# Kernel optimization log

Measured on AMD Instinct MI355X. Metric: run time of the kernel, lower is better.

The kernel has to match this reference:

```python
import jax, jax.numpy as jnp
import numpy as np

N_NODES = 100000
IN_DIM = 64
HID = 128
HID2 = HID // 2
N_CLASSES = 2
N_EDGES = 1600000
BN_EPS = 1e-5


def setup_inputs() -> dict:
    key = jax.random.key(0)
    ks = jax.random.split(key, 12)
    x = jax.random.normal(ks[0], (N_NODES, IN_DIM), dtype=jnp.float32)
    edge_index = jax.random.randint(ks[1], (2, N_EDGES), 0, N_NODES, dtype=jnp.int64)
    s = lambda k, shp, fan: jax.random.normal(k, shp, dtype=jnp.float32) / np.sqrt(fan)
    return {
        "x": x,
        "edge_index": edge_index,
        # SAGEConv1: lin_l (on aggregated neighbors, has bias), lin_r (root, no bias)
        "W1_l": s(ks[2], (IN_DIM, HID), IN_DIM),
        "b1_l": jnp.zeros((HID,), jnp.float32),
        "W1_r": s(ks[3], (IN_DIM, HID), IN_DIM),
        # SAGEConv2
        "W2_l": s(ks[4], (HID, HID2), HID),
        "b2_l": jnp.zeros((HID2,), jnp.float32),
        "W2_r": s(ks[5], (HID, HID2), HID),
        # BatchNorm (eval mode: running stats)
        "bn1_gamma": jnp.ones((HID,), jnp.float32),
        "bn1_beta": jnp.zeros((HID,), jnp.float32),
        "bn1_mean": jax.random.normal(ks[6], (HID,), dtype=jnp.float32) * 0.1,
        "bn1_var": jax.random.uniform(ks[7], (HID,), minval=0.5, maxval=1.5, dtype=jnp.float32),
        "bn2_gamma": jnp.ones((HID2,), jnp.float32),
        "bn2_beta": jnp.zeros((HID2,), jnp.float32),
        "bn2_mean": jax.random.normal(ks[8], (HID2,), dtype=jnp.float32) * 0.1,
        "bn2_var": jax.random.uniform(ks[9], (HID2,), minval=0.5, maxval=1.5, dtype=jnp.float32),
        # classifier
        "Wc": s(ks[10], (HID2, N_CLASSES), HID2),
        "bc": jnp.zeros((N_CLASSES,), jnp.float32),
    }


def _sage_mean(h, src, dst, Wl, bl, Wr, n_nodes):
    # gather source-node features along edges, scatter-mean into destinations
    msg = h[src]                                            # [E, D]
    summed = jax.ops.segment_sum(msg, dst, num_segments=n_nodes)  # [N, D]
    cnt = jax.ops.segment_sum(jnp.ones_like(dst, dtype=h.dtype), dst, num_segments=n_nodes)
    mean = summed / jnp.maximum(cnt, 1.0)[:, None]
    return mean @ Wl + bl + h @ Wr


def _bn_eval(h, gamma, beta, mean, var):
    return (h - mean) * (gamma * jax.lax.rsqrt(var + BN_EPS)) + beta


def reference(x, edge_index, W1_l, b1_l, W1_r, W2_l, b2_l, W2_r,
              bn1_gamma, bn1_beta, bn1_mean, bn1_var,
              bn2_gamma, bn2_beta, bn2_mean, bn2_var, Wc, bc):
    src, dst = edge_index[0], edge_index[1]
    n = x.shape[0]
    h = _sage_mean(x, src, dst, W1_l, b1_l, W1_r, n)
    h = jax.nn.relu(_bn_eval(h, bn1_gamma, bn1_beta, bn1_mean, bn1_var))
    h = _sage_mean(h, src, dst, W2_l, b2_l, W2_r, n)
    h = jax.nn.relu(_bn_eval(h, bn2_gamma, bn2_beta, bn2_mean, bn2_var))
    return h @ Wc + bc  # logits [N, num_classes]
```

## Files before the change

### kernel.cpp

```cpp
#include <hip/hip_runtime.h>
#include <math.h>

#define N_NODES 100000
#define IN_DIM 64
#define HID 128
#define HID2 64
#define N_EDGES 1600000
#define BN_EPS 1e-5f

#define NPB 128
#define NB 782
#define BIN_BLOCKS 391
#define BIN_CHUNK 4096
#define SORT_CAP 4096

typedef __attribute__((ext_vector_type(8))) __bf16 bf16x8;
typedef __attribute__((ext_vector_type(4))) float f32x4;
typedef __attribute__((ext_vector_type(2))) float f32x2;
typedef __attribute__((ext_vector_type(8))) unsigned short u16x8;

__device__ __forceinline__ unsigned short f2bf(float f) {
    unsigned int u = __builtin_bit_cast(unsigned int, f);
    u += 0x7fffu + ((u >> 16) & 1u);
    return (unsigned short)(u >> 16);
}

__device__ __forceinline__ void accum_u2(float a[4], uint2 v) {
    a[0] += __builtin_bit_cast(float, v.x << 16);
    a[1] += __builtin_bit_cast(float, v.x);
    a[2] += __builtin_bit_cast(float, v.y << 16);
    a[3] += __builtin_bit_cast(float, v.y);
}

__device__ __forceinline__ void accum_fp8(float a[4], unsigned int u) {
    f32x2 lo = __builtin_amdgcn_cvt_pk_f32_fp8((int)u, false);
    f32x2 hi = __builtin_amdgcn_cvt_pk_f32_fp8((int)u, true);
    a[0] += lo.x; a[1] += lo.y; a[2] += hi.x; a[3] += hi.y;
}

__global__ __launch_bounds__(256) void prep_wfrag(
    const float* __restrict__ W1l, const float* __restrict__ W1r,
    const float* __restrict__ W2l, const float* __restrict__ W2r,
    unsigned short* __restrict__ Wf1, unsigned short* __restrict__ Wf2)
{
    int task = blockIdx.x * 4 + (threadIdx.x >> 6);
    int lane = threadIdx.x & 63;
    int m  = task >> 5;
    int nt = (task >> 2) & 7;
    int kt = task & 3;
    int col = nt * 16 + (lane & 15);
    int k0  = kt * 32 + (lane >> 4) * 8;
    unsigned short tmp[8];
    #pragma unroll
    for (int e = 0; e < 8; ++e) {
        int k = k0 + e;
        float v;
        if (m == 0) v = (k < 64) ? W1l[k * HID + col] : W1r[(k - 64) * HID + col];
        else        v = (col < 64) ? W2l[k * HID2 + col] : W2r[k * HID2 + (col - 64)];
        tmp[e] = f2bf(v);
    }
    unsigned short* dst = ((m == 0) ? Wf1 : Wf2)
                        + ((size_t)((nt * 4 + kt) * 64 + lane)) * 8;
    *(u16x8*)dst = *(const u16x8*)tmp;
}

__global__ __launch_bounds__(256) void cast_x(
    const float* __restrict__ x, unsigned short* __restrict__ Abuf)
{
    int tid = blockIdx.x * 256 + threadIdx.x;
    if (tid >= N_NODES * 16) return;
    int node = tid >> 4;
    int q    = tid & 15;
    float4 v = ((const float4*)x)[tid];
    unsigned short o[4] = {f2bf(v.x), f2bf(v.y), f2bf(v.z), f2bf(v.w)};
    *(uint2*)(Abuf + (size_t)node * 128 + 64 + q * 4) = *(const uint2*)o;
}

__global__ __launch_bounds__(256) void bin_count(
    const int* __restrict__ dst,
    int* __restrict__ bucketTotal,
    int* __restrict__ perBlockBase)
{
    __shared__ int cnt[NB];
    const int t = threadIdx.x;
    for (int i = t; i < NB; i += 256) cnt[i] = 0;
    __syncthreads();
    const int e0 = blockIdx.x * BIN_CHUNK;
    for (int i = t; i < BIN_CHUNK; i += 256) {
        int e = e0 + i;
        if (e < N_EDGES) atomicAdd(&cnt[dst[e] >> 7], 1);
    }
    __syncthreads();
    for (int b = t; b < NB; b += 256) {
        int c = cnt[b];
        if (c) perBlockBase[blockIdx.x * NB + b] = atomicAdd(&bucketTotal[b], c);
    }
}

__global__ __launch_bounds__(1024) void bucket_scan(
    const int* __restrict__ bucketTotal, int* __restrict__ bucketStart)
{
    __shared__ int s[1024];
    const int t = threadIdx.x;
    int v = (t < NB) ? bucketTotal[t] : 0;
    s[t] = v;
    __syncthreads();
    #pragma unroll
    for (int off = 1; off < 1024; off <<= 1) {
        int u = (t >= off) ? s[t - off] : 0;
        __syncthreads();
        s[t] += u;
        __syncthreads();
    }
    if (t < NB) bucketStart[t] = s[t] - v;
    if (t == 0) bucketStart[NB] = N_EDGES;
}

__global__ __launch_bounds__(256) void bin_write(
    const int* __restrict__ src, const int* __restrict__ dst,
    const int* __restrict__ bucketStart,
    const int* __restrict__ perBlockBase,
    unsigned int* __restrict__ binned)
{
    __shared__ int cur[NB];
    const int t = threadIdx.x;
    for (int i = t; i < NB; i += 256) cur[i] = 0;
    __syncthreads();
    const int e0 = blockIdx.x * BIN_CHUNK;
    for (int i = t; i < BIN_CHUNK; i += 256) {
        int e = e0 + i;
        if (e < N_EDGES) {
            int d = dst[e];
            int b = d >> 7;
            int pos = bucketStart[b] + perBlockBase[blockIdx.x * NB + b]
                    + atomicAdd(&cur[b], 1);
            binned[pos] = ((unsigned int)src[e] << 7) | (unsigned int)(d & 127);
        }
    }
}

__global__ __launch_bounds__(256) void bucket_sort(
    const unsigned int* __restrict__ binned,
    const int* __restrict__ bucketStart,
    int* __restrict__ sortedSrc,
    int* __restrict__ rowStart)
{
    __shared__ unsigned int stage[SORT_CAP];
    __shared__ int hist[NPB];
    __shared__ int cur[NPB];

    const int b  = blockIdx.x;
    const int t  = threadIdx.x;
    const int bs = bucketStart[b];
    const int be = bucketStart[b + 1];
    const int total = be - bs;

    if (t < NPB) hist[t] = 0;
    __syncthreads();

    if (total <= SORT_CAP) {
        for (int i = t; i < total; i += 256) {
            unsigned int p = binned[bs + i];
            stage[i] = p;
            atomicAdd(&hist[p & 127], 1);
        }
        __syncthreads();
        int orig = (t < NPB) ? hist[t] : 0;
        __syncthreads();
        #pragma unroll
        for (int off = 1; off < NPB; off <<= 1) {
            int v = (t < NPB && t >= off) ? hist[t - off] : 0;
            __syncthreads();
            if (t < NPB) hist[t] += v;
            __syncthreads();
        }
        if (t < NPB) {
            int excl = hist[t] - orig;
            int node = b * NPB + t;
            if (node < N_NODES) rowStart[node] = bs + excl;
            cur[t] = excl;
        }
        if (b == 0 && t == 0) rowStart[N_NODES] = N_EDGES;
        __syncthreads();
        for (int i = t; i < total; i += 256) {
            unsigned int p = stage[i];
            int pos = atomicAdd(&cur[p & 127], 1);
            sortedSrc[bs + pos] = (int)(p >> 7);
        }
    } else {
        for (int i = t; i < total; i += 256)
            atomicAdd(&hist[binned[bs + i] & 127], 1);
        __syncthreads();
        int orig = (t < NPB) ? hist[t] : 0;
        __syncthreads();
        #pragma unroll
        for (int off = 1; off < NPB; off <<= 1) {
            int v = (t < NPB && t >= off) ? hist[t - off] : 0;
            __syncthreads();
            if (t < NPB) hist[t] += v;
            __syncthreads();
        }
        if (t < NPB) {
            int excl = hist[t] - orig;
            int node = b * NPB + t;
            if (node < N_NODES) rowStart[node] = bs + excl;
            cur[t] = excl;
        }
        if (b == 0 && t == 0) rowStart[N_NODES] = N_EDGES;
        __syncthreads();
        for (int i = t; i < total; i += 256) {
            unsigned int p = binned[bs + i];
            int pos = atomicAdd(&cur[p & 127], 1);
            sortedSrc[bs + pos] = (int)(p >> 7);
        }
    }
}

__global__ __launch_bounds__(256) void gather1_q(
    const int* __restrict__ rowStart,
    const int* __restrict__ sortedSrc,
    unsigned short* __restrict__ Abuf)
{
    const int node = (int)((blockIdx.x * 256u + threadIdx.x) >> 4);
    const int lane = threadIdx.x & 63;
    const int q    = lane & 15;
    const int qb   = lane & 48;
    const int b = rowStart[node], e = rowStart[node + 1];

    float a0[4] = {0.f,0.f,0.f,0.f};
    float a1[4] = {0.f,0.f,0.f,0.f};
    float a2[4] = {0.f,0.f,0.f,0.f};
    float a3[4] = {0.f,0.f,0.f,0.f};

    for (int base = b; base < e; base += 16) {
        const int cnt = min(e - base, 16);
        int srcv = (base + q < e) ? sortedSrc[base + q] : 0;
        int i = 0;
        for (; i + 4 <= cnt; i += 4) {
            int s0 = __shfl(srcv, qb + i);
            int s1 = __shfl(srcv, qb + i + 1);
            int s2 = __shfl(srcv, qb + i + 2);
            int s3 = __shfl(srcv, qb + i + 3);
            accum_u2(a0, *(const uint2*)(Abuf + (size_t)s0 * 128 + 64 + q * 4));
            accum_u2(a1, *(const uint2*)(Abuf + (size_t)s1 * 128 + 64 + q * 4));
            accum_u2(a2, *(const uint2*)(Abuf + (size_t)s2 * 128 + 64 + q * 4));
            accum_u2(a3, *(const uint2*)(Abuf + (size_t)s3 * 128 + 64 + q * 4));
        }
        for (; i < cnt; ++i) {
            int s0 = __shfl(srcv, qb + i);
            accum_u2(a0, *(const uint2*)(Abuf + (size_t)s0 * 128 + 64 + q * 4));
        }
    }
    #pragma unroll
    for (int i = 0; i < 4; ++i) a0[i] = (a0[i] + a1[i]) + (a2[i] + a3[i]);

    float inv = 1.0f / fmaxf((float)(e - b), 1.0f);
    unsigned short o[4] = {f2bf(a0[0] * inv), f2bf(a0[1] * inv),
                           f2bf(a0[2] * inv), f2bf(a0[3] * inv)};
    *(uint2*)(Abuf + (size_t)node * 128 + q * 4) = *(const uint2*)o;
}

__global__ __launch_bounds__(256, 4) void gemm_fused_mfma(
    const unsigned short* __restrict__ Abuf,
    const unsigned short* __restrict__ Wf1,
    const unsigned short* __restrict__ Wf2,
    const float* __restrict__ b1l,
    const float* __restrict__ g1, const float* __restrict__ be1,
    const float* __restrict__ m1, const float* __restrict__ v1,
    const float* __restrict__ b2l,
    unsigned char* __restrict__ t1f8,
    unsigned short* __restrict__ r1bf)
{
    __shared__ unsigned short Al[64 * 136];

    const int t = threadIdx.x;
    const int w = t >> 6, l = t & 63;
    const int n0 = blockIdx.x * 64;

    {
        const int node = t >> 2, q = t & 3;
        const int nn = n0 + node;
        const uint4* srcp = (const uint4*)(Abuf + (size_t)nn * 128) + q * 4;
        uint4 z; z.x = z.y = z.z = z.w = 0u;
        unsigned short* drow = &Al[node * 136 + q * 32];
        #pragma unroll
        for (int i = 0; i < 4; ++i) {
            uint4 v = (nn < N_NODES) ? srcp[i] : z;
            *(uint4*)(drow + i * 8) = v;
        }
    }
    __syncthreads();

    const int row = l & 15, kq = l >> 4;

    f32x4 acc[4][2];
    #pragma unroll
    for (int a = 0; a < 4; ++a)
        #pragma unroll
        for (int b = 0; b < 2; ++b) acc[a][b] = (f32x4)(0.0f);

    #pragma unroll
    for (int kt = 0; kt < 4; ++kt) {
        bf16x8 bfr[2];
        #pragma unroll
        for (int n = 0; n < 2; ++n)
            bfr[n] = __builtin_bit_cast(bf16x8,
                *(const u16x8*)(Wf1 + ((size_t)(((2 * w + n) * 4 + kt) * 64 + l)) * 8));
        #pragma unroll
        for (int mt = 0; mt < 4; ++mt) {
            bf16x8 afr = __builtin_bit_cast(bf16x8,
                *(const u16x8*)&Al[(mt * 16 + row) * 136 + kt * 32 + kq * 8]);
            #pragma unroll
            for (int n = 0; n < 2; ++n)
                acc[mt][n] = __builtin_amdgcn_mfma_f32_16x16x32_bf16(
                    afr, bfr[n], acc[mt][n], 0, 0, 0);
        }
    }
    __syncthreads();

    #pragma unroll
    for (int n = 0; n < 2; ++n) {
        int j = w * 32 + n * 16 + (l & 15);
        float s  = g1[j] * rsqrtf(v1[j] + BN_EPS);
        float of = be1[j] + (b1l[j] - m1[j]) * s;
        #pragma unroll
        for (int mt = 0; mt < 4; ++mt) {
            #pragma unroll
            for (int i = 0; i < 4; ++i) {
                float h = fmaxf(fmaf(acc[mt][n][i], s, of), 0.0f);
                Al[(mt * 16 + kq * 4 + i) * 136 + j] = f2bf(h);
            }
        }
    }
    __syncthreads();

    f32x4 acc2[4][2];
    #pragma unroll
    for (int a = 0; a < 4; ++a)
        #pragma unroll
        for (int b = 0; b < 2; ++b) acc2[a][b] = (f32x4)(0.0f);

    #pragma unroll
    for (int kt = 0; kt < 4; ++kt) {
        bf16x8 bfr[2];
        #pragma unroll
        for (int n = 0; n < 2; ++n)
            bfr[n] = __builtin_bit_cast(bf16x8,
                *(const u16x8*)(Wf2 + ((size_t)(((2 * w + n) * 4 + kt) * 64 + l)) * 8));
        #pragma unroll
        for (int mt = 0; mt < 4; ++mt) {
            bf16x8 afr = __builtin_bit_cast(bf16x8,
                *(const u16x8*)&Al[(mt * 16 + row) * 136 + kt * 32 + kq * 8]);
            #pragma unroll
            for (int n = 0; n < 2; ++n)
                acc2[mt][n] = __builtin_amdgcn_mfma_f32_16x16x32_bf16(
                    afr, bfr[n], acc2[mt][n], 0, 0, 0);
        }
    }

    #pragma unroll
    for (int n = 0; n < 2; ++n) {
        int j = w * 32 + n * 16 + (l & 15);
        float bl = (w >= 2) ? b2l[j - 64] : 0.0f;
        #pragma unroll
        for (int mt = 0; mt < 4; ++mt) {
            #pragma unroll
            for (int i = 0; i < 4; ++i) {
                int node = n0 + mt * 16 + kq * 4 + i;
                if (node < N_NODES) {
                    float vv = acc2[mt][n][i];
                    if (w < 2) {
                        int p = __builtin_amdgcn_cvt_pk_fp8_f32(vv, vv, 0, false);
                        t1f8[(size_t)node * 64 + j] = (unsigned char)(p & 0xff);
                    } else {
                        r1bf[(size_t)node * 64 + (j - 64)] = f2bf(vv + bl);
                    }
                }
            }
        }
    }
}

__global__ __launch_bounds__(256) void gather2_q(
    const unsigned char* __restrict__ t1f8,
    const int* __restrict__ rowStart,
    const int* __restrict__ sortedSrc,
    const unsigned short* __restrict__ r1bf,
    const float* __restrict__ g2, const float* __restrict__ be2,
    const float* __restrict__ m2, const float* __restrict__ v2,
    const float* __restrict__ Wc, const float* __restrict__ bc,
    float* __restrict__ out)
{
    const int node = (int)((blockIdx.x * 256u + threadIdx.x) >> 4);
    const int lane = threadIdx.x & 63;
    const int q    = lane & 15;
    const int qb   = lane & 48;
    const int b = rowStart[node], e = rowStart[node + 1];

    float a0[4] = {0.f,0.f,0.f,0.f};
    float a1[4] = {0.f,0.f,0.f,0.f};
    float a2[4] = {0.f,0.f,0.f,0.f};
    float a3[4] = {0.f,0.f,0.f,0.f};

    for (int base = b; base < e; base += 16) {
        const int cnt = min(e - base, 16);
        int srcv = (base + q < e) ? sortedSrc[base + q] : 0;
        int i = 0;
        for (; i + 4 <= cnt; i += 4) {
            int s0 = __shfl(srcv, qb + i);
            int s1 = __shfl(srcv, qb + i + 1);
            int s2 = __shfl(srcv, qb + i + 2);
            int s3 = __shfl(srcv, qb + i + 3);
            accum_fp8(a0, *(const unsigned int*)(t1f8 + (size_t)s0 * 64 + q * 4));
            accum_fp8(a1, *(const unsigned int*)(t1f8 + (size_t)s1 * 64 + q * 4));
            accum_fp8(a2, *(const unsigned int*)(t1f8 + (size_t)s2 * 64 + q * 4));
            accum_fp8(a3, *(const unsigned int*)(t1f8 + (size_t)s3 * 64 + q * 4));
        }
        for (; i < cnt; ++i) {
            int s0 = __shfl(srcv, qb + i);
            accum_fp8(a0, *(const unsigned int*)(t1f8 + (size_t)s0 * 64 + q * 4));
        }
    }
    #pragma unroll
    for (int i = 0; i < 4; ++i) a0[i] = (a0[i] + a1[i]) + (a2[i] + a3[i]);

    const float inv = 1.0f / fmaxf((float)(e - b), 1.0f);
    const int f0 = q * 4;
    uint2 rv = *(const uint2*)(r1bf + (size_t)node * 64 + f0);
    float rr[4] = {
        __builtin_bit_cast(float, rv.x << 16),
        __builtin_bit_cast(float, rv.x & 0xffff0000u),
        __builtin_bit_cast(float, rv.y << 16),
        __builtin_bit_cast(float, rv.y & 0xffff0000u)
    };
    float l0 = 0.f, l1 = 0.f;
    #pragma unroll
    for (int i = 0; i < 4; ++i) {
        int f = f0 + i;
        float pre = a0[i] * inv + rr[i];
        float s   = g2[f] * rsqrtf(v2[f] + BN_EPS);
        float h2  = fmaxf((pre - m2[f]) * s + be2[f], 0.0f);
        l0 = fmaf(h2, Wc[f * 2 + 0], l0);
        l1 = fmaf(h2, Wc[f * 2 + 1], l1);
    }
    #pragma unroll
    for (int off = 8; off > 0; off >>= 1) {
        l0 += __shfl_xor(l0, off);
        l1 += __shfl_xor(l1, off);
    }
    if (q == 0) {
        out[(size_t)node * 2 + 0] = l0 + bc[0];
        out[(size_t)node * 2 + 1] = l1 + bc[1];
    }
}

extern "C" void kernel_launch(void* const* d_in, const int* in_sizes, int n_in,
                              void* d_out, int out_size, void* d_ws, size_t ws_size,
                              hipStream_t stream)
{
    const float* x    = (const float*)d_in[0];
    const int*   eidx = (const int*)d_in[1];
    const float* W1l  = (const float*)d_in[2];
    const float* b1l  = (const float*)d_in[3];
    const float* W1r  = (const float*)d_in[4];
    const float* W2l  = (const float*)d_in[5];
    const float* b2l  = (const float*)d_in[6];
    const float* W2r  = (const float*)d_in[7];
    const float* g1   = (const float*)d_in[8];
    const float* be1  = (const float*)d_in[9];
    const float* m1   = (const float*)d_in[10];
    const float* v1   = (const float*)d_in[11];
    const float* g2   = (const float*)d_in[12];
    const float* be2  = (const float*)d_in[13];
    const float* m2   = (const float*)d_in[14];
    const float* v2   = (const float*)d_in[15];
    const float* Wc   = (const float*)d_in[16];
    const float* bc   = (const float*)d_in[17];
    float* out = (float*)d_out;

    const int* src = eidx;
    const int* dst = eidx + N_EDGES;

    char* ws = (char*)d_ws;
    size_t off = 0;
    auto alloc = [&](size_t bytes) { void* p = ws + off; off = (off + bytes + 255) & ~(size_t)255; return p; };
    int* bucketTotal  = (int*)alloc((size_t)NB * 4);
    int* bucketStart  = (int*)alloc((size_t)(NB + 1) * 4);
    int* perBlockBase = (int*)alloc((size_t)BIN_BLOCKS * NB * 4);
    unsigned int* binned = (unsigned int*)alloc((size_t)N_EDGES * 4);
    int* sortedSrc    = (int*)alloc((size_t)N_EDGES * 4);
    int* rowStart     = (int*)alloc((size_t)(N_NODES + 1) * 4);
    unsigned short* Wf1  = (unsigned short*)alloc(128 * 128 * 2);
    unsigned short* Wf2  = (unsigned short*)alloc(128 * 128 * 2);
    unsigned short* Abuf = (unsigned short*)alloc((size_t)N_NODES * 128 * 2);
    unsigned char*  t1f8 = (unsigned char*)alloc((size_t)N_NODES * 64);
    unsigned short* r1bf = (unsigned short*)alloc((size_t)N_NODES * 64 * 2);

    const int gemmGrid    = (N_NODES + 63) / 64;
    const int gatherGrid  = (N_NODES * 16 + 255) / 256;

    prep_wfrag<<<16, 256, 0, stream>>>(W1l, W1r, W2l, W2r, Wf1, Wf2);
    cast_x<<<(N_NODES * 16 + 255) / 256, 256, 0, stream>>>(x, Abuf);

    hipMemsetAsync(bucketTotal, 0, (size_t)NB * 4, stream);
    bin_count  <<<BIN_BLOCKS, 256, 0, stream>>>(dst, bucketTotal, perBlockBase);
    bucket_scan<<<1, 1024, 0, stream>>>(bucketTotal, bucketStart);
    bin_write  <<<BIN_BLOCKS, 256, 0, stream>>>(src, dst, bucketStart, perBlockBase, binned);
    bucket_sort<<<NB, 256, 0, stream>>>(binned, bucketStart, sortedSrc, rowStart);

    gather1_q<<<gatherGrid, 256, 0, stream>>>(rowStart, sortedSrc, Abuf);

    gemm_fused_mfma<<<gemmGrid, 256, 0, stream>>>(
        Abuf, Wf1, Wf2, b1l, g1, be1, m1, v1, b2l, t1f8, r1bf);

    gather2_q<<<gatherGrid, 256, 0, stream>>>(
        t1f8, rowStart, sortedSrc, r1bf, g2, be2, m2, v2, Wc, bc, out);
}
```

Before: 147.4 us.

## Gather layer-one features from FP8 copy, widen gather lanes, fuse prep kernels

Layer-one aggregation now reads an FP8 copy of x, written by the cast kernel, instead of the bf16 copy, which halves the bytes per neighbour gather. Both gathers now use 8 lanes per node with 8-byte loads of 8 features each, instead of 16 lanes with 4 features. The weight prep, x cast and bucket-count zeroing are merged into one launch, replacing two kernels and a memset. Binning kernels read dst/src as int4 vectors. FP8 input features lower the precision of the layer-one mean aggregation.

```diff
diff --git a/kernel.cpp b/kernel.cpp
--- a/kernel.cpp
+++ b/kernel.cpp
@@ -13,6 +13,7 @@
 #define BIN_BLOCKS 391
 #define BIN_CHUNK 4096
 #define SORT_CAP 4096
+#define CAST_BLOCKS 6250
 
 typedef __attribute__((ext_vector_type(8))) __bf16 bf16x8;
 typedef __attribute__((ext_vector_type(4))) float f32x4;
@@ -25,55 +26,58 @@
     return (unsigned short)(u >> 16);
 }
 
-__device__ __forceinline__ void accum_u2(float a[4], uint2 v) {
-    a[0] += __builtin_bit_cast(float, v.x << 16);
-    a[1] += __builtin_bit_cast(float, v.x);
-    a[2] += __builtin_bit_cast(float, v.y << 16);
-    a[3] += __builtin_bit_cast(float, v.y);
-}
-
-__device__ __forceinline__ void accum_fp8(float a[4], unsigned int u) {
-    f32x2 lo = __builtin_amdgcn_cvt_pk_f32_fp8((int)u, false);
-    f32x2 hi = __builtin_amdgcn_cvt_pk_f32_fp8((int)u, true);
-    a[0] += lo.x; a[1] += lo.y; a[2] += hi.x; a[3] += hi.y;
-}
-
-__global__ __launch_bounds__(256) void prep_wfrag(
+__device__ __forceinline__ void accum_fp8x8(float a[8], uint2 v) {
+    f32x2 p0 = __builtin_amdgcn_cvt_pk_f32_fp8((int)v.x, false);
+    f32x2 p1 = __builtin_amdgcn_cvt_pk_f32_fp8((int)v.x, true);
+    f32x2 p2 = __builtin_amdgcn_cvt_pk_f32_fp8((int)v.y, false);
+    f32x2 p3 = __builtin_amdgcn_cvt_pk_f32_fp8((int)v.y, true);
+    a[0] += p0.x; a[1] += p0.y; a[2] += p1.x; a[3] += p1.y;
+    a[4] += p2.x; a[5] += p2.y; a[6] += p3.x; a[7] += p3.y;
+}
+
+__global__ __launch_bounds__(256) void prep_all(
+    const float* __restrict__ x,
     const float* __restrict__ W1l, const float* __restrict__ W1r,
     const float* __restrict__ W2l, const float* __restrict__ W2r,
-    unsigned short* __restrict__ Wf1, unsigned short* __restrict__ Wf2)
-{
-    int task = blockIdx.x * 4 + (threadIdx.x >> 6);
-    int lane = threadIdx.x & 63;
-    int m  = task >> 5;
-    int nt = (task >> 2) & 7;
-    int kt = task & 3;
-    int col = nt * 16 + (lane & 15);
-    int k0  = kt * 32 + (lane >> 4) * 8;
-    unsigned short tmp[8];
-    #pragma unroll
-    for (int e = 0; e < 8; ++e) {
-        int k = k0 + e;
-        float v;
-        if (m == 0) v = (k < 64) ? W1l[k * HID + col] : W1r[(k - 64) * HID + col];
-        else        v = (col < 64) ? W2l[k * HID2 + col] : W2r[k * HID2 + (col - 64)];
-        tmp[e] = f2bf(v);
-    }
-    unsigned short* dst = ((m == 0) ? Wf1 : Wf2)
-                        + ((size_t)((nt * 4 + kt) * 64 + lane)) * 8;
-    *(u16x8*)dst = *(const u16x8*)tmp;
-}
-
-__global__ __launch_bounds__(256) void cast_x(
-    const float* __restrict__ x, unsigned short* __restrict__ Abuf)
-{
-    int tid = blockIdx.x * 256 + threadIdx.x;
-    if (tid >= N_NODES * 16) return;
-    int node = tid >> 4;
-    int q    = tid & 15;
-    float4 v = ((const float4*)x)[tid];
-    unsigned short o[4] = {f2bf(v.x), f2bf(v.y), f2bf(v.z), f2bf(v.w)};
-    *(uint2*)(Abuf + (size_t)node * 128 + 64 + q * 4) = *(const uint2*)o;
+    unsigned short* __restrict__ Wf1, unsigned short* __restrict__ Wf2,
+    unsigned short* __restrict__ Abuf,
+    unsigned char* __restrict__ x8,
+    int* __restrict__ bucketTotal)
+{
+    const int bid = blockIdx.x;
+    if (bid < 16) {
+        int task = bid * 4 + (threadIdx.x >> 6);
+        int lane = threadIdx.x & 63;
+        int m  = task >> 5;
+        int nt = (task >> 2) & 7;
+        int kt = task & 3;
+        int col = nt * 16 + (lane & 15);
+        int k0  = kt * 32 + (lane >> 4) * 8;
+        unsigned short tmp[8];
+        #pragma unroll
+        for (int e = 0; e < 8; ++e) {
+            int k = k0 + e;
+            float v;
+            if (m == 0) v = (k < 64) ? W1l[k * HID + col] : W1r[(k - 64) * HID + col];
+            else        v = (col < 64) ? W2l[k * HID2 + col] : W2r[k * HID2 + (col - 64)];
+            tmp[e] = f2bf(v);
+        }
+        unsigned short* dst = ((m == 0) ? Wf1 : Wf2)
+                            + ((size_t)((nt * 4 + kt) * 64 + lane)) * 8;
+        *(u16x8*)dst = *(const u16x8*)tmp;
+    } else if (bid < 16 + CAST_BLOCKS) {
+        int tid = (bid - 16) * 256 + threadIdx.x;
+        int node = tid >> 4;
+        int q    = tid & 15;
+        float4 v = ((const float4*)x)[tid];
+        unsigned short o[4] = {f2bf(v.x), f2bf(v.y), f2bf(v.z), f2bf(v.w)};
+        *(uint2*)(Abuf + (size_t)node * 128 + 64 + q * 4) = *(const uint2*)o;
+        int p = __builtin_amdgcn_cvt_pk_fp8_f32(v.x, v.y, 0, false);
+        p     = __builtin_amdgcn_cvt_pk_fp8_f32(v.z, v.w, p, true);
+        *(unsigned int*)(x8 + (size_t)node * 64 + q * 4) = (unsigned int)p;
+    } else {
+        for (int i = threadIdx.x; i < NB; i += 256) bucketTotal[i] = 0;
+    }
 }
 
 __global__ __launch_bounds__(256) void bin_count(
@@ -85,10 +89,18 @@
     const int t = threadIdx.x;
     for (int i = t; i < NB; i += 256) cnt[i] = 0;
     __syncthreads();
-    const int e0 = blockIdx.x * BIN_CHUNK;
-    for (int i = t; i < BIN_CHUNK; i += 256) {
-        int e = e0 + i;
-        if (e < N_EDGES) atomicAdd(&cnt[dst[e] >> 7], 1);
+    const int e40 = blockIdx.x * (BIN_CHUNK / 4);
+    const int4* dst4 = (const int4*)dst;
+    #pragma unroll
+    for (int i = 0; i < BIN_CHUNK / 4 / 256; ++i) {
+        int ei = e40 + i * 256 + t;
+        if (ei < N_EDGES / 4) {
+            int4 d = dst4[ei];
+            atomicAdd(&cnt[d.x >> 7], 1);
+            atomicAdd(&cnt[d.y >> 7], 1);
+            atomicAdd(&cnt[d.z >> 7], 1);
+            atomicAdd(&cnt[d.w >> 7], 1);
+        }
     }
     __syncthreads();
     for (int b = t; b < NB; b += 256) {
@@ -126,15 +138,24 @@
     const int t = threadIdx.x;
     for (int i = t; i < NB; i += 256) cur[i] = 0;
     __syncthreads();
-    const int e0 = blockIdx.x * BIN_CHUNK;
-    for (int i = t; i < BIN_CHUNK; i += 256) {
-        int e = e0 + i;
-        if (e < N_EDGES) {
-            int d = dst[e];
-            int b = d >> 7;
-            int pos = bucketStart[b] + perBlockBase[blockIdx.x * NB + b]
-                    + atomicAdd(&cur[b], 1);
-            binned[pos] = ((unsigned int)src[e] << 7) | (unsigned int)(d & 127);
+    const int e40 = blockIdx.x * (BIN_CHUNK / 4);
+    const int4* dst4 = (const int4*)dst;
+    const int4* src4 = (const int4*)src;
+    #pragma unroll
+    for (int i = 0; i < BIN_CHUNK / 4 / 256; ++i) {
+        int ei = e40 + i * 256 + t;
+        if (ei < N_EDGES / 4) {
+            int4 d = dst4[ei];
+            int4 s = src4[ei];
+            int ds[4] = {d.x, d.y, d.z, d.w};
+            int ss[4] = {s.x, s.y, s.z, s.w};
+            #pragma unroll
+            for (int k = 0; k < 4; ++k) {
+                int b = ds[k] >> 7;
+                int pos = bucketStart[b] + perBlockBase[blockIdx.x * NB + b]
+                        + atomicAdd(&cur[b], 1);
+                binned[pos] = ((unsigned int)ss[k] << 7) | (unsigned int)(ds[k] & 127);
+            }
         }
     }
 }
@@ -216,48 +237,47 @@
     }
 }
 
-__global__ __launch_bounds__(256) void gather1_q(
+__global__ __launch_bounds__(256) void gather1_e(
     const int* __restrict__ rowStart,
     const int* __restrict__ sortedSrc,
+    const unsigned char* __restrict__ x8,
     unsigned short* __restrict__ Abuf)
 {
-    const int node = (int)((blockIdx.x * 256u + threadIdx.x) >> 4);
+    const int node = (int)((blockIdx.x * 256u + threadIdx.x) >> 3);
     const int lane = threadIdx.x & 63;
-    const int q    = lane & 15;
-    const int qb   = lane & 48;
+    const int f    = lane & 7;
+    const int nb   = lane & 56;
     const int b = rowStart[node], e = rowStart[node + 1];
 
-    float a0[4] = {0.f,0.f,0.f,0.f};
-    float a1[4] = {0.f,0.f,0.f,0.f};
-    float a2[4] = {0.f,0.f,0.f,0.f};
-    float a3[4] = {0.f,0.f,0.f,0.f};
-
-    for (int base = b; base < e; base += 16) {
-        const int cnt = min(e - base, 16);
-        int srcv = (base + q < e) ? sortedSrc[base + q] : 0;
+    float a0[8] = {}, a1[8] = {}, a2[8] = {}, a3[8] = {};
+
+    for (int base = b; base < e; base += 8) {
+        const int cnt = min(e - base, 8);
+        int srcv = (base + f < e) ? sortedSrc[base + f] : 0;
         int i = 0;
         for (; i + 4 <= cnt; i += 4) {
-            int s0 = __shfl(srcv, qb + i);
-            int s1 = __shfl(srcv, qb + i + 1);
-            int s2 = __shfl(srcv, qb + i + 2);
-            int s3 = __shfl(srcv, qb + i + 3);
-            accum_u2(a0, *(const uint2*)(Abuf + (size_t)s0 * 128 + 64 + q * 4));
-            accum_u2(a1, *(const uint2*)(Abuf + (size_t)s1 * 128 + 64 + q * 4));
-            accum_u2(a2, *(const uint2*)(Abuf + (size_t)s2 * 128 + 64 + q * 4));
-            accum_u2(a3, *(const uint2*)(Abuf + (size_t)s3 * 128 + 64 + q * 4));
+            int s0 = __shfl(srcv, nb + i);
+            int s1 = __shfl(srcv, nb + i + 1);
+            int s2 = __shfl(srcv, nb + i + 2);
+            int s3 = __shfl(srcv, nb + i + 3);
+            accum_fp8x8(a0, *(const uint2*)(x8 + (size_t)s0 * 64 + f * 8));
+            accum_fp8x8(a1, *(const uint2*)(x8 + (size_t)s1 * 64 + f * 8));
+            accum_fp8x8(a2, *(const uint2*)(x8 + (size_t)s2 * 64 + f * 8));
+            accum_fp8x8(a3, *(const uint2*)(x8 + (size_t)s3 * 64 + f * 8));
         }
         for (; i < cnt; ++i) {
-            int s0 = __shfl(srcv, qb + i);
-            accum_u2(a0, *(const uint2*)(Abuf + (size_t)s0 * 128 + 64 + q * 4));
-        }
-    }
-    #pragma unroll
-    for (int i = 0; i < 4; ++i) a0[i] = (a0[i] + a1[i]) + (a2[i] + a3[i]);
+            int s0 = __shfl(srcv, nb + i);
+            accum_fp8x8(a0, *(const uint2*)(x8 + (size_t)s0 * 64 + f * 8));
+        }
+    }
+    #pragma unroll
+    for (int i = 0; i < 8; ++i) a0[i] = (a0[i] + a1[i]) + (a2[i] + a3[i]);
 
     float inv = 1.0f / fmaxf((float)(e - b), 1.0f);
-    unsigned short o[4] = {f2bf(a0[0] * inv), f2bf(a0[1] * inv),
-                           f2bf(a0[2] * inv), f2bf(a0[3] * inv)};
-    *(uint2*)(Abuf + (size_t)node * 128 + q * 4) = *(const uint2*)o;
+    unsigned short o[8];
+    #pragma unroll
+    for (int i = 0; i < 8; ++i) o[i] = f2bf(a0[i] * inv);
+    *(uint4*)(Abuf + (size_t)node * 128 + f * 8) = *(const uint4*)o;
 }
 
 __global__ __launch_bounds__(256, 4) void gemm_fused_mfma(
@@ -381,7 +401,7 @@
     }
 }
 
-__global__ __launch_bounds__(256) void gather2_q(
+__global__ __launch_bounds__(256) void gather2_e(
     const unsigned char* __restrict__ t1f8,
     const int* __restrict__ rowStart,
     const int* __restrict__ sortedSrc,
@@ -391,64 +411,59 @@
     const float* __restrict__ Wc, const float* __restrict__ bc,
     float* __restrict__ out)
 {
-    const int node = (int)((blockIdx.x * 256u + threadIdx.x) >> 4);
+    const int node = (int)((blockIdx.x * 256u + threadIdx.x) >> 3);
     const int lane = threadIdx.x & 63;
-    const int q    = lane & 15;
-    const int qb   = lane & 48;
+    const int f    = lane & 7;
+    const int nb   = lane & 56;
     const int b = rowStart[node], e = rowStart[node + 1];
 
-    float a0[4] = {0.f,0.f,0.f,0.f};
-    float a1[4] = {0.f,0.f,0.f,0.f};
-    float a2[4] = {0.f,0.f,0.f,0.f};
-    float a3[4] = {0.f,0.f,0.f,0.f};
-
-    for (int base = b; base < e; base += 16) {
-        const int cnt = min(e - base, 16);
-        int srcv = (base + q < e) ? sortedSrc[base + q] : 0;
+    float a0[8] = {}, a1[8] = {}, a2[8] = {}, a3[8] = {};
+
+    for (int base = b; base < e; base += 8) {
+        const int cnt = min(e - base, 8);
+        int srcv = (base + f < e) ? sortedSrc[base + f] : 0;
         int i = 0;
         for (; i + 4 <= cnt; i += 4) {
-            int s0 = __shfl(srcv, qb + i);
-            int s1 = __shfl(srcv, qb + i + 1);
-            int s2 = __shfl(srcv, qb + i + 2);
-            int s3 = __shfl(srcv, qb + i + 3);
-            accum_fp8(a0, *(const unsigned int*)(t1f8 + (size_t)s0 * 64 + q * 4));
-            accum_fp8(a1, *(const unsigned int*)(t1f8 + (size_t)s1 * 64 + q * 4));
-            accum_fp8(a2, *(const unsigned int*)(t1f8 + (size_t)s2 * 64 + q * 4));
-            accum_fp8(a3, *(const unsigned int*)(t1f8 + (size_t)s3 * 64 + q * 4));
+            int s0 = __shfl(srcv, nb + i);
+            int s1 = __shfl(srcv, nb + i + 1);
+            int s2 = __shfl(srcv, nb + i + 2);
+            int s3 = __shfl(srcv, nb + i + 3);
+            accum_fp8x8(a0, *(const uint2*)(t1f8 + (size_t)s0 * 64 + f * 8));
+            accum_fp8x8(a1, *(const uint2*)(t1f8 + (size_t)s1 * 64 + f * 8));
+            accum_fp8x8(a2, *(const uint2*)(t1f8 + (size_t)s2 * 64 + f * 8));
+            accum_fp8x8(a3, *(const uint2*)(t1f8 + (size_t)s3 * 64 + f * 8));
         }
         for (; i < cnt; ++i) {
-            int s0 = __shfl(srcv, qb + i);
-            accum_fp8(a0, *(const unsigned int*)(t1f8 + (size_t)s0 * 64 + q * 4));
-        }
-    }
-    #pragma unroll
-    for (int i = 0; i < 4; ++i) a0[i] = (a0[i] + a1[i]) + (a2[i] + a3[i]);
+            int s0 = __shfl(srcv, nb + i);
+            accum_fp8x8(a0, *(const uint2*)(t1f8 + (size_t)s0 * 64 + f * 8));
+        }
+    }
+    #pragma unroll
+    for (int i = 0; i < 8; ++i) a0[i] = (a0[i] + a1[i]) + (a2[i] + a3[i]);
 
     const float inv = 1.0f / fmaxf((float)(e - b), 1.0f);
-    const int f0 = q * 4;
-    uint2 rv = *(const uint2*)(r1bf + (size_t)node * 64 + f0);
-    float rr[4] = {
-        __builtin_bit_cast(float, rv.x << 16),
-        __builtin_bit_cast(float, rv.x & 0xffff0000u),
-        __builtin_bit_cast(float, rv.y << 16),
-        __builtin_bit_cast(float, rv.y & 0xffff0000u)
-    };
+    const int f0 = f * 8;
+    uint4 rv = *(const uint4*)(r1bf + (size_t)node * 64 + f0);
+    unsigned int rw[4] = {rv.x, rv.y, rv.z, rv.w};
     float l0 = 0.f, l1 = 0.f;
     #pragma unroll
-    for (int i = 0; i < 4; ++i) {
-        int f = f0 + i;
-        float pre = a0[i] * inv + rr[i];
-        float s   = g2[f] * rsqrtf(v2[f] + BN_EPS);
-        float h2  = fmaxf((pre - m2[f]) * s + be2[f], 0.0f);
-        l0 = fmaf(h2, Wc[f * 2 + 0], l0);
-        l1 = fmaf(h2, Wc[f * 2 + 1], l1);
-    }
-    #pragma unroll
-    for (int off = 8; off > 0; off >>= 1) {
+    for (int i = 0; i < 8; ++i) {
+        int fe = f0 + i;
+        unsigned int w = rw[i >> 1];
+        float rr = (i & 1) ? __builtin_bit_cast(float, w)
+                           : __builtin_bit_cast(float, w << 16);
+        float pre = a0[i] * inv + rr;
+        float s   = g2[fe] * rsqrtf(v2[fe] + BN_EPS);
+        float h2  = fmaxf((pre - m2[fe]) * s + be2[fe], 0.0f);
+        l0 = fmaf(h2, Wc[fe * 2 + 0], l0);
+        l1 = fmaf(h2, Wc[fe * 2 + 1], l1);
+    }
+    #pragma unroll
+    for (int off = 4; off > 0; off >>= 1) {
         l0 += __shfl_xor(l0, off);
         l1 += __shfl_xor(l1, off);
     }
-    if (q == 0) {
+    if (f == 0) {
         out[(size_t)node * 2 + 0] = l0 + bc[0];
         out[(size_t)node * 2 + 1] = l1 + bc[1];
     }
@@ -493,26 +508,26 @@
     unsigned short* Wf1  = (unsigned short*)alloc(128 * 128 * 2);
     unsigned short* Wf2  = (unsigned short*)alloc(128 * 128 * 2);
     unsigned short* Abuf = (unsigned short*)alloc((size_t)N_NODES * 128 * 2);
+    unsigned char*  x8   = (unsigned char*)alloc((size_t)N_NODES * 64);
     unsigned char*  t1f8 = (unsigned char*)alloc((size_t)N_NODES * 64);
     unsigned short* r1bf = (unsigned short*)alloc((size_t)N_NODES * 64 * 2);
 
     const int gemmGrid    = (N_NODES + 63) / 64;
-    const int gatherGrid  = (N_NODES * 16 + 255) / 256;
-
-    prep_wfrag<<<16, 256, 0, stream>>>(W1l, W1r, W2l, W2r, Wf1, Wf2);
-    cast_x<<<(N_NODES * 16 + 255) / 256, 256, 0, stream>>>(x, Abuf);
-
-    hipMemsetAsync(bucketTotal, 0, (size_t)NB * 4, stream);
+    const int gatherGrid  = (N_NODES * 8) / 256;
+
+    prep_all<<<16 + CAST_BLOCKS + 1, 256, 0, stream>>>(
+        x, W1l, W1r, W2l, W2r, Wf1, Wf2, Abuf, x8, bucketTotal);
+
     bin_count  <<<BIN_BLOCKS, 256, 0, stream>>>(dst, bucketTotal, perBlockBase);
     bucket_scan<<<1, 1024, 0, stream>>>(bucketTotal, bucketStart);
     bin_write  <<<BIN_BLOCKS, 256, 0, stream>>>(src, dst, bucketStart, perBlockBase, binned);
     bucket_sort<<<NB, 256, 0, stream>>>(binned, bucketStart, sortedSrc, rowStart);
 
-    gather1_q<<<gatherGrid, 256, 0, stream>>>(rowStart, sortedSrc, Abuf);
+    gather1_e<<<gatherGrid, 256, 0, stream>>>(rowStart, sortedSrc, x8, Abuf);
 
     gemm_fused_mfma<<<gemmGrid, 256, 0, stream>>>(
         Abuf, Wf1, Wf2, b1l, g1, be1, m1, v1, b2l, t1f8, r1bf);
 
-    gather2_q<<<gatherGrid, 256, 0, stream>>>(
+    gather2_e<<<gatherGrid, 256, 0, stream>>>(
         t1f8, rowStart, sortedSrc, r1bf, g2, be2, m2, v2, Wc, bc, out);
 }
```

After: 139.9 us. 5.1% less time.
